# Optimization experiments

Hardware: AMD Instinct MI355X
Metric: run time of the kernel (lower is better)

Reference implementation:

```python
import jax, jax.numpy as jnp
import numpy as np

IMG = 128
NEAR, FAR = 1.0, 100.0
BG_EPS = 1e-3      # eps in soft_rasterize: background depth logit
SIGMA = 1e-6       # sigma_val
DIST_EPS = 1e-4    # dist_eps
GAMMA = 1e-6       # gamma_val
CHUNK = 500
B, V, F = 1, 5023, 10000


def setup_inputs():
    key = jax.random.key(0)
    k1, k2, k3, k4 = jax.random.split(key, 4)
    xy = jax.random.uniform(k1, (B, V, 2), minval=-1.0, maxval=1.0, dtype=jnp.float32)
    z = jax.random.uniform(k2, (B, V, 1), minval=5.0, maxval=15.0, dtype=jnp.float32)
    vertices = jnp.concatenate([xy, z], axis=-1)              # [B,V,3]
    faces = jax.random.randint(k3, (B, F, 3), 0, V, dtype=jnp.int32)
    attributes = jax.random.uniform(k4, (B, F, 3, 3), dtype=jnp.float32)
    return {"vertices": vertices, "faces": faces, "attributes": attributes}


def _seg_dist2(px, py, ax, ay, bx, by):
    # squared distance from pixel (px,py) to segment a-b; broadcasts [P] vs [B,C,1]
    dx = px - ax; dy = py - ay
    ex = bx - ax; ey = by - ay
    l2 = jnp.maximum(ex * ex + ey * ey, 1e-12)
    t = jnp.clip((dx * ex + dy * ey) / l2, 0.0, 1.0)
    rx = dx - t * ex; ry = dy - t * ey
    return rx * rx + ry * ry


def _render(vertices, faces, attributes):
    is_ = IMG
    P = is_ * is_
    bz = vertices.shape[0]
    v = vertices.at[..., 0].multiply(-1.0)                    # x flip (in-place in torch)
    fv = jax.vmap(lambda vv, ff: vv[ff])(v, faces)            # [B,F,3vert,3xyz]
    tex = attributes[..., :3]                                 # [B,F,3vert,3rgb]
    # fill_back=True: append copies with reversed winding
    fv = jnp.concatenate([fv, fv[:, :, ::-1, :]], axis=1)     # [B,2F,3,3]
    tex = jnp.concatenate([tex, tex[:, :, ::-1, :]], axis=1)
    F2 = fv.shape[1]
    pad = (-F2) % CHUNK
    valid = jnp.concatenate([jnp.ones((F2,), bool), jnp.zeros((pad,), bool)])
    fv = jnp.pad(fv, ((0, 0), (0, pad), (0, 0), (0, 0)))
    tex = jnp.pad(tex, ((0, 0), (0, pad), (0, 0), (0, 0)))
    n_chunks = (F2 + pad) // CHUNK
    fv = jnp.transpose(fv.reshape(bz, n_chunks, CHUNK, 3, 3), (1, 0, 2, 3, 4))
    tex = jnp.transpose(tex.reshape(bz, n_chunks, CHUNK, 3, 3), (1, 0, 2, 3, 4))
    valid = valid.reshape(n_chunks, CHUNK)

    # pixel centers in [-1,1]; row 0 is the top of the image (y flipped as in CUDA)
    xs = (2.0 * jnp.arange(is_, dtype=jnp.float32) + 1.0 - is_) / is_
    ys = (2.0 * (is_ - 1 - jnp.arange(is_, dtype=jnp.float32)) + 1.0 - is_) / is_
    px = jnp.broadcast_to(xs[None, :], (is_, is_)).reshape(-1)  # [P]
    py = jnp.broadcast_to(ys[:, None], (is_, is_)).reshape(-1)

    thr = DIST_EPS * SIGMA
    inv_g = 1.0 / GAMMA

    def step(carry, inp):
        m, s, cacc, prod = carry                # [B,P],[B,P],[B,3,P],[B,P]
        fvc, txc, vld = inp                     # [B,C,3,3],[B,C,3,3],[C]
        x0 = fvc[:, :, 0, 0][..., None]; y0 = fvc[:, :, 0, 1][..., None]; z0 = fvc[:, :, 0, 2][..., None]
        x1 = fvc[:, :, 1, 0][..., None]; y1 = fvc[:, :, 1, 1][..., None]; z1 = fvc[:, :, 1, 2][..., None]
        x2 = fvc[:, :, 2, 0][..., None]; y2 = fvc[:, :, 2, 1][..., None]; z2 = fvc[:, :, 2, 2][..., None]
        det = (y1 - y2) * (x0 - x2) + (x2 - x1) * (y0 - y2)   # [B,C,1]
        det = jnp.where(jnp.abs(det) < 1e-10, jnp.where(det < 0, -1e-10, 1e-10), det)
        w0 = ((y1 - y2) * (px - x2) + (x2 - x1) * (py - y2)) / det  # [B,C,P]
        w1 = ((y2 - y0) * (px - x2) + (x0 - x2) * (py - y2)) / det
        w2 = 1.0 - w0 - w1
        inside = (w0 >= 0) & (w1 >= 0) & (w2 >= 0)
        dis = jnp.minimum(jnp.minimum(_seg_dist2(px, py, x0, y0, x1, y1),
                                      _seg_dist2(px, py, x1, y1, x2, y2)),
                          _seg_dist2(px, py, x2, y2, x0, y0))     # [B,C,P] squared dist
        contrib = (inside | (dis < thr)) & vld[None, :, None]
        sgn = jnp.where(inside, 1.0, -1.0)
        Dp = jnp.where(contrib, jax.nn.sigmoid(sgn * dis / SIGMA), 0.0)
        prod = prod * jnp.prod(1.0 - Dp, axis=1)                  # alpha: prod(1-D)
        # clipped barycentric + perspective-correct depth
        c0 = jnp.clip(w0, 0.0, 1.0); c1 = jnp.clip(w1, 0.0, 1.0); c2 = jnp.clip(w2, 0.0, 1.0)
        csum = jnp.maximum(c0 + c1 + c2, 1e-5)
        c0 = c0 / csum; c1 = c1 / csum; c2 = c2 / csum
        zp_inv = c0 / z0 + c1 / z1 + c2 / z2
        zp = 1.0 / jnp.where(jnp.abs(zp_inv) < 1e-12, 1e-12, zp_inv)
        front = (y2 - y0) * (x1 - x0) < (y1 - y0) * (x2 - x0)     # [B,C,1]
        rgb_m = contrib & front & (zp >= NEAR) & (zp <= FAR)
        zpn = (FAR - zp) / (FAR - NEAR)
        new_m = jnp.maximum(m, jnp.max(jnp.where(rgb_m, zpn, -jnp.inf), axis=1))
        e = jnp.exp(jnp.where(rgb_m, (zpn - new_m[:, None, :]) * inv_g, -jnp.inf)) * Dp
        scale = jnp.exp((m - new_m) * inv_g)                      # [B,P]
        wc = jnp.stack([c0, c1, c2], axis=2)                      # [B,C,3,P]
        col = jnp.einsum('bcvp,bcvk->bckp', wc, txc)              # interpolated rgb
        s = s * scale + jnp.sum(e, axis=1)
        cacc = cacc * scale[:, None, :] + jnp.sum(e[:, :, None, :] * col, axis=1)
        return (new_m, s, cacc, prod), None

    m0 = jnp.full((bz, P), BG_EPS, jnp.float32)   # background logit = eps
    s0 = jnp.ones((bz, P), jnp.float32)           # exp((eps - m0)/gamma) = 1
    c0_ = jnp.zeros((bz, 3, P), jnp.float32)      # black background
    p0 = jnp.ones((bz, P), jnp.float32)
    (m, s, cacc, prod), _ = jax.lax.scan(jax.checkpoint(step), (m0, s0, c0_, p0), (fv, tex, valid))
    rgb = cacc / s[:, None, :]
    alpha = 1.0 - prod
    return jnp.concatenate([rgb, alpha[:, None, :]], axis=1).reshape(bz, 4, is_, is_)


def reference(vertices, faces, attributes):
    return _render(vertices, faces, attributes)
```

## Files before the change

kernel.cpp:

```cpp
#include <hip/hip_runtime.h>
#include <math.h>


#define NFACE 10000
#define IMG   128
#define P_TOT (IMG*IMG)
#define FSTR  40
#define NTILE 64
#define NQ    4
#define CAPQ  2500
#define CAP   (CAPQ*NQ)
#define BMAX  4096
#define NB    1024
#define CH    256
#define NCH   40
#define Z_LO  0.85f
#define Z_W   (0.12f/1024.0f)

__device__ __forceinline__ float rcp_nr(float x) {
    float r = __builtin_amdgcn_rcpf(x);
    r = r * __builtin_fmaf(-x, r, 2.0f);
    return r;
}

__device__ __forceinline__ float segd(float px, float py, float ax, float ay,
                                      float bx, float by, float il) {
    float dx = px - ax, dy = py - ay;
    float ex = bx - ax, ey = by - ay;
    float t = (dx * ex + dy * ey) * il;
    t = fminf(fmaxf(t, 0.0f), 1.0f);
    float rx = dx - t * ex, ry = dy - t * ey;
    return rx * rx + ry * ry;
}

__device__ __forceinline__ float rfl_f(float x) {
    return __uint_as_float(__builtin_amdgcn_readfirstlane(__float_as_uint(x)));
}

__device__ __forceinline__ int zbucket(float zub) {
    int b = (int)((zub - Z_LO) * (1.0f / Z_W));
    return min(max(b, 0), NB - 1);
}

__global__ __launch_bounds__(256) void k_prehist(const float* __restrict__ v,
                                                 const int* __restrict__ fc,
                                                 const float* __restrict__ at,
                                                 float* __restrict__ fb,
                                                 int* __restrict__ hist) {
    __shared__ int lh[NB];
    int c = blockIdx.x, tid = threadIdx.x;
    for (int j = tid; j < NB; j += 256) lh[j] = 0;
    __syncthreads();

    int f = c * CH + tid;
    if (f < NFACE) {
        int i0 = fc[3 * f], i1 = fc[3 * f + 1], i2 = fc[3 * f + 2];
        float x0 = -v[3 * i0], y0 = v[3 * i0 + 1], z0 = v[3 * i0 + 2];
        float x1 = -v[3 * i1], y1 = v[3 * i1 + 1], z1 = v[3 * i1 + 2];
        float x2 = -v[3 * i2], y2 = v[3 * i2 + 1], z2 = v[3 * i2 + 2];

        float det = (y1 - y2) * (x0 - x2) + (x2 - x1) * (y0 - y2);
        if (fabsf(det) < 1e-10f) det = (det < 0.0f) ? -1e-10f : 1e-10f;
        float a0 = y1 - y2, b0 = x2 - x1, a1 = y2 - y0, b1 = x0 - x2, detp = det;
        if (det < 0.0f) { detp = -det; a0 = -a0; b0 = -b0; a1 = -a1; b1 = -b1; }

        float a2 = a0 + a1, b2 = b0 + b1;
        float g0 = fmaxf(sqrtf(a0 * a0 + b0 * b0), 1e-12f);
        float g1 = fmaxf(sqrtf(a1 * a1 + b1 * b1), 1e-12f);
        float g2 = fmaxf(sqrtf(a2 * a2 + b2 * b2), 1e-12f);
        const float MARG = 3e-5f, AG = 1e-9f;
        float m0 = -(MARG * g0 + AG), m1 = -(MARG * g1 + AG), m2 = -(MARG * g2 + AG);

        float e01x = x1 - x0, e01y = y1 - y0;
        float e12x = x2 - x1, e12y = y2 - y1;
        float e20x = x0 - x2, e20y = y0 - y2;
        float il01 = 1.0f / fmaxf(e01x * e01x + e01y * e01y, 1e-12f);
        float il12 = 1.0f / fmaxf(e12x * e12x + e12y * e12y, 1e-12f);
        float il20 = 1.0f / fmaxf(e20x * e20x + e20y * e20y, 1e-12f);

        const float BM = 2e-5f;
        float bxmin = fminf(fminf(x0, x1), x2) - BM, bxmax = fmaxf(fmaxf(x0, x1), x2) + BM;
        float bymin = fminf(fminf(y0, y1), y2) - BM, bymax = fmaxf(fmaxf(y0, y1), y2) + BM;

        int mult = (((y2 - y0) * (x1 - x0)) < ((y1 - y0) * (x2 - x0)))
                 + (((y0 - y2) * (x1 - x2)) < ((y1 - y2) * (x0 - x2)));

        float zmin = fminf(fminf(z0, z1), z2);
        float zub = (100.0f - zmin) / 99.0f + 2e-6f;

        float* F = fb + (size_t)f * FSTR;
        F[0] = bxmin; F[1] = bxmax; F[2] = bymin; F[3] = bymax;
        F[4] = x2; F[5] = y2; F[6] = a0; F[7] = b0;
        F[8] = a1; F[9] = b1; F[10] = detp; F[11] = zub;
        F[12] = m0; F[13] = m1; F[14] = m2; F[15] = (float)mult;
        F[16] = x0; F[17] = y0; F[18] = x1; F[19] = y1;
        F[20] = il01; F[21] = il12; F[22] = il20; F[23] = 1.0f / detp;
        F[24] = 1.0f / z0; F[25] = 1.0f / z1; F[26] = 1.0f / z2;
        F[27] = 1.0f / g0; F[28] = 1.0f / g1; F[29] = 1.0f / g2;
#pragma unroll
        for (int k = 0; k < 9; k++) F[30 + k] = at[(size_t)f * 9 + k];
        F[39] = 0.0f;

        atomicAdd(&lh[zbucket(zub)], 1);
    }
    __syncthreads();
    for (int j = tid; j < NB; j += 256) hist[c * NB + j] = lh[j];
}

__global__ __launch_bounds__(1024) void k_scan(int* __restrict__ hist) {
    __shared__ int a[NB];
    int t = threadIdx.x;
    int tot = 0;
    for (int c = 0; c < NCH; c++) tot += hist[c * NB + t];
    a[t] = tot;
    for (int off = 1; off < NB; off <<= 1) {
        __syncthreads();
        int v = a[t] + ((t + off < NB) ? a[t + off] : 0);
        __syncthreads();
        a[t] = v;
    }
    int r = a[t] - tot;
    for (int c = 0; c < NCH; c++) {
        int h = hist[c * NB + t];
        hist[c * NB + t] = r;
        r += h;
    }
}

__global__ __launch_bounds__(256) void k_scatterre(const float* __restrict__ fb,
                                                   const int* __restrict__ hist,
                                                   float* __restrict__ fb2) {
    __shared__ int sb[CH];
    int c = blockIdx.x, tid = threadIdx.x;
    int f = c * CH + tid;
    bool valid = (f < NFACE);
    int b = valid ? zbucket(fb[(size_t)f * FSTR + 11]) : -1;
    sb[tid] = b;
    __syncthreads();
    if (valid) {
        int rank = 0;
        for (int j = 0; j < CH; j++) {
            int v2 = sb[j];
            rank += (j < tid && v2 == b) ? 1 : 0;
        }
        int pos = hist[c * NB + b] + rank;
        const float4* src = (const float4*)(fb + (size_t)f * FSTR);
        float4* dst = (float4*)(fb2 + (size_t)pos * FSTR);
#pragma unroll
        for (int k = 0; k < 10; k++) dst[k] = src[k];
        fb2[(size_t)pos * FSTR + 11] = Z_LO + (float)(b + 1) * Z_W + 1e-7f;
    }
}

__global__ __launch_bounds__(256) void k_bin(const float* __restrict__ fb2,
                                             float2* __restrict__ tmeta,
                                             int* __restrict__ cnt4) {
    int t = blockIdx.x >> 2, q = blockIdx.x & 3;
    int tid = threadIdx.x, wv = tid >> 6, lane = tid & 63;
    int tx = t & 7, ty = t >> 3;
    float x_lo = (float)(2 * (tx * 16) + 1 - IMG) / (float)IMG;
    float x_hi = (float)(2 * (tx * 16 + 15) + 1 - IMG) / (float)IMG;
    float y_hi = (float)(127 - 2 * (ty * 16)) / (float)IMG;
    float y_lo = (float)(127 - 2 * (ty * 16 + 15)) / (float)IMG;
    float cx = 0.5f * (x_lo + x_hi), hx = 0.5f * (x_hi - x_lo);
    float cy = 0.5f * (y_lo + y_hi), hy = 0.5f * (y_hi - y_lo);

    __shared__ int wc[4];
    int cnt = 0;
    int f0 = q * CAPQ;
    for (int base = f0; base < f0 + CAPQ; base += 256) {
        int j = base + tid;
        bool ov = false;
        float zub = 0.0f;
        if (j < f0 + CAPQ) {
            const float4* H = (const float4*)(fb2 + (size_t)j * FSTR);
            float4 h0 = H[0], h1 = H[1], h2 = H[2], h3 = H[3];
            ov = (h0.x <= x_hi) & (h0.y >= x_lo) & (h0.z <= y_hi) & (h0.w >= y_lo);
            if (ov) {
                float dx = cx - h1.x, dy = cy - h1.y;
                float mx0 = h1.z * dx + h1.w * dy + fabsf(h1.z) * hx + fabsf(h1.w) * hy;
                float mx1 = h2.x * dx + h2.y * dy + fabsf(h2.x) * hx + fabsf(h2.y) * hy;
                float A2 = -(h1.z + h2.x), B2 = -(h1.w + h2.y);
                float mx2 = h2.z + A2 * dx + B2 * dy + fabsf(A2) * hx + fabsf(B2) * hy;
                ov = (mx0 >= h3.x) & (mx1 >= h3.y) & (mx2 >= h3.z);
                zub = h2.w;
            }
        }
        unsigned long long mask = __ballot(ov);
        if (lane == 0) wc[wv] = __popcll(mask);
        __syncthreads();
        int off = cnt;
        for (int w = 0; w < 4; ++w) {
            if (w < wv) off += wc[w];
        }
        if (ov) {
            int pos = off + __popcll(mask & ((1ull << lane) - 1ull));
            tmeta[(size_t)t * CAP + q * CAPQ + pos] =
                make_float2(zub, __int_as_float(j));
        }
        cnt += wc[0] + wc[1] + wc[2] + wc[3];
        __syncthreads();
    }
    if (tid == 0) cnt4[t * 4 + q] = cnt;
}

__global__ __launch_bounds__(64) void k_map(const int* __restrict__ cnt4,
                                            int* __restrict__ map,
                                            int* __restrict__ starts,
                                            int* __restrict__ segs,
                                            int B) {
    int lane = threadIdx.x;
    int len = cnt4[4 * lane] + cnt4[4 * lane + 1] + cnt4[4 * lane + 2] + cnt4[4 * lane + 3];
    int tot = len;
    for (int o = 32; o > 0; o >>= 1) tot += __shfl_down(tot, o);
    tot = __shfl(tot, 0);
    int St = max(1, (int)(((long long)len * (long long)(B - NTILE)) /
                          (long long)max(tot, 1)));
    __shared__ int sS[64], sP[64];
    sS[lane] = St;
    __syncthreads();
    if (lane == 0) {
        int acc = 0;
        for (int t = 0; t < 64; ++t) { sP[t] = acc; acc += sS[t]; }
    }
    __syncthreads();
    for (int i = lane; i < B; i += 64) map[i] = -1;
    __syncthreads();
    int st = sP[lane];
    starts[lane] = st;
    segs[lane] = St;
    for (int s = 0; s < St; ++s) map[st + s] = (lane << 16) | s;
}

__global__ __launch_bounds__(256) void k_main(const float* __restrict__ fb2,
                                              const float2* __restrict__ tmeta,
                                              const int* __restrict__ cnt4,
                                              const int* __restrict__ map,
                                              const int* __restrict__ segs,
                                              float* __restrict__ part) {
    int bid = blockIdx.x;
    int mv = map[bid];
    if (mv < 0) return;
    int t = mv >> 16, seg = mv & 0xffff;
    int S = segs[t];

    int tid = threadIdx.x;
    int tx = t & 7, ty = t >> 3;
    int col = tx * 16 + (tid & 15);
    int row = ty * 16 + (tid >> 4);
    float px = (float)(2 * col + 1 - IMG) / (float)IMG;
    float py = (float)(2 * (IMG - 1 - row) + 1 - IMG) / (float)IMG;

    const float2* pm = tmeta + (size_t)t * CAP;

    float m = -__builtin_inff();
    float s = 0.0f, ca = 0.0f, cb = 0.0f, cc = 0.0f, pr = 1.0f;

    const float NEAR_T = 4.3e-3f;
    const float ZM = 1.3e-4f;

    bool done = false;
    for (int q = 0; q < 4 && !done; ++q) {
        int qlen = cnt4[t * 4 + q];
        for (int i = seg; i < qlen; i += S) {
            float2 mt = pm[q * CAPQ + i];
            float zcur = rfl_f(mt.x);
            if (__all((pr == 0.0f) & (zcur <= m - ZM))) { done = true; break; }
            int fj = __builtin_amdgcn_readfirstlane(__float_as_int(mt.y));
            const float4* H = (const float4*)(fb2 + (size_t)fj * FSTR);
            float4 g0 = H[0], g1 = H[1], g2 = H[2], g3 = H[3];

            bool inbox = (px >= g0.x) & (px <= g0.y) & (py >= g0.z) & (py <= g0.w);
            if (!__any(inbox)) continue;

            float x2 = g1.x, y2 = g1.y;
            float dx2 = px - x2, dy2 = py - y2;
            float num0 = g1.z * dx2 + g1.w * dy2;
            float num1 = g2.x * dx2 + g2.y * dy2;
            float detp = g2.z;
            float num2 = detp - num0 - num1;
            bool maybe = inbox & (num0 >= g3.x) & (num1 >= g3.y) & (num2 >= g3.z);
            if (!__any(maybe)) continue;

            const float* F = fb2 + (size_t)fj * FSTR;

            bool inside = (num0 >= 0.0f) & (num1 >= 0.0f) & (num2 >= 0.0f);
            bool inside_l = inside & inbox;

            float lin0 = num0 * F[27];
            float lin1 = num1 * F[28];
            float lin2 = num2 * F[29];
            float lbmin = fminf(fminf(lin0, lin1), lin2);

            bool outNear = maybe & (!inside);
            bool nearIn  = inside_l & (lbmin < NEAR_T);
            bool anyNear = __any(nearIn | outNear);

            float dis = 1e9f;
            float Dp;
            if (anyNear) {
                bool needAll = __any(outNear);
                float x0 = F[16], y0 = F[17], x1 = F[18], y1 = F[19];
                float d01 = 1e9f, d12 = 1e9f, d20 = 1e9f;
                if (needAll | __any(inside_l & (lin2 < NEAR_T)))
                    d01 = segd(px, py, x0, y0, x1, y1, F[20]);
                if (needAll | __any(inside_l & (lin0 < NEAR_T)))
                    d12 = segd(px, py, x1, y1, x2, y2, F[21]);
                if (needAll | __any(inside_l & (lin1 < NEAR_T)))
                    d20 = segd(px, py, x2, y2, x0, y0, F[22]);
                dis = fminf(fminf(d01, d12), d20);

                float qq = dis * 1e6f;
                float xs_ = inside ? qq : -qq;
                float tt = __expf(-fabsf(xs_));
                float Dpn = (xs_ >= 0.0f ? 1.0f : tt) * rcp_nr(1.0f + tt);
                bool nearl = nearIn | outNear;
                Dp = nearl ? Dpn : (inside_l ? 1.0f : 0.0f);
            } else {
                Dp = inside_l ? 1.0f : 0.0f;
            }

            bool contrib = inside_l | (outNear & (dis < 1e-10f));
            Dp = contrib ? Dp : 0.0f;
            float omd = 1.0f - Dp;
            pr *= contrib ? (omd * omd) : 1.0f;

            float multf = g3.w;
            bool doz = contrib & (multf > 0.0f);
            if (__any(doz & (zcur > m - ZM))) {
                float rdetp = F[23];
                float w0 = num0 * rdetp;
                float w1 = num1 * rdetp;
                float c0 = fminf(fmaxf(w0, 0.0f), 1.0f);
                float c1 = fminf(fmaxf(w1, 0.0f), 1.0f);
                float c2 = fminf(fmaxf(1.0f - w0 - w1, 0.0f), 1.0f);
                float csum = fmaxf(c0 + c1 + c2, 1e-5f);
                float rcs = rcp_nr(csum);
                c0 *= rcs; c1 *= rcs; c2 *= rcs;
                float zpi = c0 * F[24] + c1 * F[25] + c2 * F[26];
                if (fabsf(zpi) < 1e-12f) zpi = 1e-12f;
                float zp = rcp_nr(zpi);
                if (doz & (zp >= 1.0f) & (zp <= 100.0f)) {
                    float zpn = (100.0f - zp) / 99.0f;
                    if (zpn > m) {
                        float scl = __expf((m - zpn) * 1e6f);
                        s *= scl; ca *= scl; cb *= scl; cc *= scl;
                        m = zpn;
                    }
                    float arg = (zpn - m) * 1e6f;
                    if (arg > -110.0f) {
                        float e = __expf(arg) * Dp * multf;
                        float col0 = c0 * F[30] + c1 * F[33] + c2 * F[36];
                        float col1 = c0 * F[31] + c1 * F[34] + c2 * F[37];
                        float col2 = c0 * F[32] + c1 * F[35] + c2 * F[38];
                        s += e; ca += e * col0; cb += e * col1; cc += e * col2;
                    }
                }
            }
        }
    }

    size_t pb = (size_t)bid * 6 * 256;
    part[pb + 0 * 256 + tid] = m;
    part[pb + 1 * 256 + tid] = s;
    part[pb + 2 * 256 + tid] = ca;
    part[pb + 3 * 256 + tid] = cb;
    part[pb + 4 * 256 + tid] = cc;
    part[pb + 5 * 256 + tid] = pr;
}

__global__ __launch_bounds__(1024) void k_reduce(const float* __restrict__ part,
                                                 const int* __restrict__ starts,
                                                 const int* __restrict__ segs,
                                                 float* __restrict__ out) {
    __shared__ float sm[4][256], ss[4][256], sa[4][256], sb2[4][256],
                     sc[4][256], sp[4][256];
    int t = blockIdx.x;
    int tid = threadIdx.x;
    int q = tid & 255, sub = tid >> 8;
    int start = starts[t], S = segs[t];

    const float NINF = -__builtin_inff();
    float mp = NINF;
    for (int sgi = sub; sgi < S; sgi += 4)
        mp = fmaxf(mp, part[((size_t)(start + sgi) * 6 + 0) * 256 + q]);
    float sum = 0.0f, a = 0.0f, b = 0.0f, c = 0.0f, pr = 1.0f;
    for (int sgi = sub; sgi < S; sgi += 4) {
        const float* r = part + ((size_t)(start + sgi) * 6) * 256;
        float rm = r[0 * 256 + q];
        float w = (rm == NINF) ? 0.0f : __expf((rm - mp) * 1e6f);
        pr *= r[5 * 256 + q];
        if (__any(w != 0.0f)) {
            sum += r[1 * 256 + q] * w;
            a += r[2 * 256 + q] * w;
            b += r[3 * 256 + q] * w;
            c += r[4 * 256 + q] * w;
        }
    }
    sm[sub][q] = mp; ss[sub][q] = sum; sa[sub][q] = a;
    sb2[sub][q] = b; sc[sub][q] = c;  sp[sub][q] = pr;
    __syncthreads();
    if (sub == 0) {
        int tx = t & 7, ty = t >> 3;
        int col = tx * 16 + (q & 15);
        int row = ty * 16 + (q >> 4);
        int p = row * IMG + col;
        float M = 0.001f;
#pragma unroll
        for (int k = 0; k < 4; k++) M = fmaxf(M, sm[k][q]);
        float SUM = __expf((0.001f - M) * 1e6f);
        float A = 0.0f, B2 = 0.0f, C = 0.0f, PR = 1.0f;
#pragma unroll
        for (int k = 0; k < 4; k++) {
            float w = __expf((sm[k][q] - M) * 1e6f);
            SUM += ss[k][q] * w;
            A += sa[k][q] * w;
            B2 += sb2[k][q] * w;
            C += sc[k][q] * w;
            PR *= sp[k][q];
        }
        out[0 * P_TOT + p] = A / SUM;
        out[1 * P_TOT + p] = B2 / SUM;
        out[2 * P_TOT + p] = C / SUM;
        out[3 * P_TOT + p] = 1.0f - PR;
    }
}

extern "C" void kernel_launch(void* const* d_in, const int* in_sizes, int n_in,
                              void* d_out, int out_size, void* d_ws, size_t ws_size,
                              hipStream_t stream) {
    const float* verts = (const float*)d_in[0];
    const int*   faces = (const int*)d_in[1];
    const float* attrs = (const float*)d_in[2];
    float* out = (float*)d_out;
    float* ws  = (float*)d_ws;

    float*  fb    = ws;
    int*    hist  = (int*)(fb + (size_t)NFACE * FSTR);
    float*  fb2   = (float*)(hist + NCH * NB);
    float2* tmeta = (float2*)(fb2 + (size_t)NFACE * FSTR);
    int*    cnt4  = (int*)(tmeta + (size_t)NTILE * CAP);
    int*    map   = cnt4 + NTILE * 4;
    int*    starts= map + BMAX;
    int*    segs  = starts + NTILE;
    float*  part  = (float*)(segs + NTILE);

    size_t used_f = 2 * (size_t)NFACE * FSTR + NCH * NB
                  + 2 * (size_t)NTILE * CAP + NTILE * 4 + BMAX + 2 * NTILE;
    long   rem_f  = (long)(ws_size / 4) - (long)used_f;
    int B = (int)(rem_f / (6 * 256));
    if (B > BMAX) B = BMAX;
    if (B < 256)  B = 256;

    k_prehist<<<NCH, 256, 0, stream>>>(verts, faces, attrs, fb, hist);
    k_scan<<<1, 1024, 0, stream>>>(hist);
    k_scatterre<<<NCH, 256, 0, stream>>>(fb, hist, fb2);
    k_bin<<<NTILE * NQ, 256, 0, stream>>>(fb2, tmeta, cnt4);
    k_map<<<1, 64, 0, stream>>>(cnt4, map, starts, segs, B);
    k_main<<<B, 256, 0, stream>>>(fb2, tmeta, cnt4, map, segs, part);
    k_reduce<<<NTILE, 1024, 0, stream>>>(part, starts, segs, out);
}
```

Before: 139.1 us.

## Fold tile map into main/reduce, unroll face loop by two, use 8x8 wave pixel blocks

Drops the separate k_map launch. k_main and k_reduce now each rebuild the tile-to-block map in shared memory from the bin counts and find their tile with a binary search. The face loop now loads two faces' headers ahead of evaluating them, to hide global-load latency. Each wave now covers an 8x8 pixel square instead of four 16-pixel rows, so wave-level early-exit and ballot tests work on more compact regions. The cost is redundant map computation in every block plus higher register pressure from the two prefetched headers.

```diff
diff --git a/kernel.cpp b/kernel.cpp
--- a/kernel.cpp
+++ b/kernel.cpp
@@ -204,50 +204,51 @@
     if (tid == 0) cnt4[t * 4 + q] = cnt;
 }
 
-__global__ __launch_bounds__(64) void k_map(const int* __restrict__ cnt4,
-                                            int* __restrict__ map,
-                                            int* __restrict__ starts,
-                                            int* __restrict__ segs,
-                                            int B) {
-    int lane = threadIdx.x;
-    int len = cnt4[4 * lane] + cnt4[4 * lane + 1] + cnt4[4 * lane + 2] + cnt4[4 * lane + 3];
-    int tot = len;
-    for (int o = 32; o > 0; o >>= 1) tot += __shfl_down(tot, o);
-    tot = __shfl(tot, 0);
-    int St = max(1, (int)(((long long)len * (long long)(B - NTILE)) /
-                          (long long)max(tot, 1)));
-    __shared__ int sS[64], sP[64];
-    sS[lane] = St;
-    __syncthreads();
-    if (lane == 0) {
+__device__ __forceinline__ void derive_map(const int* __restrict__ cnt4,
+                                           int B, int tid, int nthr,
+                                           int* sLen, int* sS, int* sP,
+                                           int* sUsed) {
+    if (tid < NTILE)
+        sLen[tid] = cnt4[4 * tid] + cnt4[4 * tid + 1]
+                  + cnt4[4 * tid + 2] + cnt4[4 * tid + 3];
+    __syncthreads();
+    if (tid == 0) {
+        int tot = 0;
+        for (int k = 0; k < NTILE; k++) tot += sLen[k];
+        tot = max(tot, 1);
         int acc = 0;
-        for (int t = 0; t < 64; ++t) { sP[t] = acc; acc += sS[t]; }
-    }
-    __syncthreads();
-    for (int i = lane; i < B; i += 64) map[i] = -1;
-    __syncthreads();
-    int st = sP[lane];
-    starts[lane] = st;
-    segs[lane] = St;
-    for (int s = 0; s < St; ++s) map[st + s] = (lane << 16) | s;
+        for (int k = 0; k < NTILE; k++) {
+            int S = max(1, (int)(((long long)sLen[k] * (long long)(B - NTILE)) /
+                                 (long long)tot));
+            sS[k] = S; sP[k] = acc; acc += S;
+        }
+        *sUsed = acc;
+    }
+    __syncthreads();
 }
 
 __global__ __launch_bounds__(256) void k_main(const float* __restrict__ fb2,
                                               const float2* __restrict__ tmeta,
                                               const int* __restrict__ cnt4,
-                                              const int* __restrict__ map,
-                                              const int* __restrict__ segs,
-                                              float* __restrict__ part) {
+                                              float* __restrict__ part,
+                                              int B) {
+    __shared__ int sLen[NTILE], sS[NTILE], sP[NTILE], sUsed;
+    int tid = threadIdx.x;
+    derive_map(cnt4, B, tid, 256, sLen, sS, sP, &sUsed);
     int bid = blockIdx.x;
-    int mv = map[bid];
-    if (mv < 0) return;
-    int t = mv >> 16, seg = mv & 0xffff;
-    int S = segs[t];
-
-    int tid = threadIdx.x;
+    if (bid >= sUsed) return;
+    int lo = 0, hi = NTILE - 1;
+    while (lo < hi) {
+        int mid = (lo + hi + 1) >> 1;
+        if (sP[mid] <= bid) lo = mid; else hi = mid - 1;
+    }
+    int t = lo, seg = bid - sP[lo];
+    int S = sS[t];
+
+    int wv = tid >> 6, lane = tid & 63;
     int tx = t & 7, ty = t >> 3;
-    int col = tx * 16 + (tid & 15);
-    int row = ty * 16 + (tid >> 4);
+    int col = tx * 16 + (wv & 1) * 8 + (lane & 7);
+    int row = ty * 16 + (wv >> 1) * 8 + (lane >> 3);
     float px = (float)(2 * col + 1 - IMG) / (float)IMG;
     float py = (float)(2 * (IMG - 1 - row) + 1 - IMG) / (float)IMG;
 
@@ -258,166 +259,188 @@
 
     const float NEAR_T = 4.3e-3f;
     const float ZM = 1.3e-4f;
+
+    auto EVAL = [&](int fj, float zcur, float4 g0, float4 g1, float4 g2, float4 g3) {
+        bool inbox = (px >= g0.x) & (px <= g0.y) & (py >= g0.z) & (py <= g0.w);
+        if (!__any(inbox)) return;
+
+        float x2 = g1.x, y2 = g1.y;
+        float dx2 = px - x2, dy2 = py - y2;
+        float num0 = g1.z * dx2 + g1.w * dy2;
+        float num1 = g2.x * dx2 + g2.y * dy2;
+        float detp = g2.z;
+        float num2 = detp - num0 - num1;
+        bool maybe = inbox & (num0 >= g3.x) & (num1 >= g3.y) & (num2 >= g3.z);
+        if (!__any(maybe)) return;
+
+        const float* F = fb2 + (size_t)fj * FSTR;
+
+        bool inside = (num0 >= 0.0f) & (num1 >= 0.0f) & (num2 >= 0.0f);
+        bool inside_l = inside & inbox;
+
+        float lin0 = num0 * F[27];
+        float lin1 = num1 * F[28];
+        float lin2 = num2 * F[29];
+        float lbmin = fminf(fminf(lin0, lin1), lin2);
+
+        bool outNear = maybe & (!inside);
+        bool nearIn  = inside_l & (lbmin < NEAR_T);
+        bool anyNear = __any(nearIn | outNear);
+
+        float dis = 1e9f;
+        float Dp;
+        if (anyNear) {
+            bool needAll = __any(outNear);
+            float x0 = F[16], y0 = F[17], x1 = F[18], y1 = F[19];
+            float d01 = 1e9f, d12 = 1e9f, d20 = 1e9f;
+            if (needAll | __any(inside_l & (lin2 < NEAR_T)))
+                d01 = segd(px, py, x0, y0, x1, y1, F[20]);
+            if (needAll | __any(inside_l & (lin0 < NEAR_T)))
+                d12 = segd(px, py, x1, y1, x2, y2, F[21]);
+            if (needAll | __any(inside_l & (lin1 < NEAR_T)))
+                d20 = segd(px, py, x2, y2, x0, y0, F[22]);
+            dis = fminf(fminf(d01, d12), d20);
+
+            float qq = dis * 1e6f;
+            float xs_ = inside ? qq : -qq;
+            float tt = __expf(-fabsf(xs_));
+            float Dpn = (xs_ >= 0.0f ? 1.0f : tt) * rcp_nr(1.0f + tt);
+            bool nearl = nearIn | outNear;
+            Dp = nearl ? Dpn : (inside_l ? 1.0f : 0.0f);
+        } else {
+            Dp = inside_l ? 1.0f : 0.0f;
+        }
+
+        bool contrib = inside_l | (outNear & (dis < 1e-10f));
+        Dp = contrib ? Dp : 0.0f;
+        float omd = 1.0f - Dp;
+        pr *= contrib ? (omd * omd) : 1.0f;
+
+        float multf = g3.w;
+        bool doz = contrib & (multf > 0.0f);
+        if (__any(doz & (zcur > m - ZM))) {
+            float rdetp = F[23];
+            float w0 = num0 * rdetp;
+            float w1 = num1 * rdetp;
+            float c0 = fminf(fmaxf(w0, 0.0f), 1.0f);
+            float c1 = fminf(fmaxf(w1, 0.0f), 1.0f);
+            float c2 = fminf(fmaxf(1.0f - w0 - w1, 0.0f), 1.0f);
+            float csum = fmaxf(c0 + c1 + c2, 1e-5f);
+            float rcs = rcp_nr(csum);
+            c0 *= rcs; c1 *= rcs; c2 *= rcs;
+            float zpi = c0 * F[24] + c1 * F[25] + c2 * F[26];
+            if (fabsf(zpi) < 1e-12f) zpi = 1e-12f;
+            float zp = rcp_nr(zpi);
+            if (doz & (zp >= 1.0f) & (zp <= 100.0f)) {
+                float zpn = (100.0f - zp) / 99.0f;
+                if (zpn > m) {
+                    float scl = __expf((m - zpn) * 1e6f);
+                    s *= scl; ca *= scl; cb *= scl; cc *= scl;
+                    m = zpn;
+                }
+                float arg = (zpn - m) * 1e6f;
+                if (arg > -110.0f) {
+                    float e = __expf(arg) * Dp * multf;
+                    float col0 = c0 * F[30] + c1 * F[33] + c2 * F[36];
+                    float col1 = c0 * F[31] + c1 * F[34] + c2 * F[37];
+                    float col2 = c0 * F[32] + c1 * F[35] + c2 * F[38];
+                    s += e; ca += e * col0; cb += e * col1; cc += e * col2;
+                }
+            }
+        }
+    };
 
     bool done = false;
     for (int q = 0; q < 4 && !done; ++q) {
         int qlen = cnt4[t * 4 + q];
-        for (int i = seg; i < qlen; i += S) {
-            float2 mt = pm[q * CAPQ + i];
-            float zcur = rfl_f(mt.x);
-            if (__all((pr == 0.0f) & (zcur <= m - ZM))) { done = true; break; }
-            int fj = __builtin_amdgcn_readfirstlane(__float_as_int(mt.y));
-            const float4* H = (const float4*)(fb2 + (size_t)fj * FSTR);
-            float4 g0 = H[0], g1 = H[1], g2 = H[2], g3 = H[3];
-
-            bool inbox = (px >= g0.x) & (px <= g0.y) & (py >= g0.z) & (py <= g0.w);
-            if (!__any(inbox)) continue;
-
-            float x2 = g1.x, y2 = g1.y;
-            float dx2 = px - x2, dy2 = py - y2;
-            float num0 = g1.z * dx2 + g1.w * dy2;
-            float num1 = g2.x * dx2 + g2.y * dy2;
-            float detp = g2.z;
-            float num2 = detp - num0 - num1;
-            bool maybe = inbox & (num0 >= g3.x) & (num1 >= g3.y) & (num2 >= g3.z);
-            if (!__any(maybe)) continue;
-
-            const float* F = fb2 + (size_t)fj * FSTR;
-
-            bool inside = (num0 >= 0.0f) & (num1 >= 0.0f) & (num2 >= 0.0f);
-            bool inside_l = inside & inbox;
-
-            float lin0 = num0 * F[27];
-            float lin1 = num1 * F[28];
-            float lin2 = num2 * F[29];
-            float lbmin = fminf(fminf(lin0, lin1), lin2);
-
-            bool outNear = maybe & (!inside);
-            bool nearIn  = inside_l & (lbmin < NEAR_T);
-            bool anyNear = __any(nearIn | outNear);
-
-            float dis = 1e9f;
-            float Dp;
-            if (anyNear) {
-                bool needAll = __any(outNear);
-                float x0 = F[16], y0 = F[17], x1 = F[18], y1 = F[19];
-                float d01 = 1e9f, d12 = 1e9f, d20 = 1e9f;
-                if (needAll | __any(inside_l & (lin2 < NEAR_T)))
-                    d01 = segd(px, py, x0, y0, x1, y1, F[20]);
-                if (needAll | __any(inside_l & (lin0 < NEAR_T)))
-                    d12 = segd(px, py, x1, y1, x2, y2, F[21]);
-                if (needAll | __any(inside_l & (lin1 < NEAR_T)))
-                    d20 = segd(px, py, x2, y2, x0, y0, F[22]);
-                dis = fminf(fminf(d01, d12), d20);
-
-                float qq = dis * 1e6f;
-                float xs_ = inside ? qq : -qq;
-                float tt = __expf(-fabsf(xs_));
-                float Dpn = (xs_ >= 0.0f ? 1.0f : tt) * rcp_nr(1.0f + tt);
-                bool nearl = nearIn | outNear;
-                Dp = nearl ? Dpn : (inside_l ? 1.0f : 0.0f);
-            } else {
-                Dp = inside_l ? 1.0f : 0.0f;
+        const float2* pq = pm + q * CAPQ;
+        int i = seg;
+        while (i < qlen) {
+            float2 mt0 = pq[i];
+            int i1 = i + S;
+            bool has1 = (i1 < qlen);
+            float2 mt1 = has1 ? pq[i1] : mt0;
+            float z0 = rfl_f(mt0.x);
+            int   f0 = __builtin_amdgcn_readfirstlane(__float_as_int(mt0.y));
+            float z1 = rfl_f(mt1.x);
+            int   f1 = __builtin_amdgcn_readfirstlane(__float_as_int(mt1.y));
+            const float4* H0 = (const float4*)(fb2 + (size_t)f0 * FSTR);
+            const float4* H1 = (const float4*)(fb2 + (size_t)f1 * FSTR);
+            float4 a0 = H0[0], a1 = H0[1], a2 = H0[2], a3 = H0[3];
+            float4 b0 = H1[0], b1 = H1[1], b2 = H1[2], b3 = H1[3];
+
+            if (__all((pr == 0.0f) & (z0 <= m - ZM))) { done = true; break; }
+            EVAL(f0, z0, a0, a1, a2, a3);
+            if (has1) {
+                if (__all((pr == 0.0f) & (z1 <= m - ZM))) { done = true; break; }
+                EVAL(f1, z1, b0, b1, b2, b3);
             }
-
-            bool contrib = inside_l | (outNear & (dis < 1e-10f));
-            Dp = contrib ? Dp : 0.0f;
-            float omd = 1.0f - Dp;
-            pr *= contrib ? (omd * omd) : 1.0f;
-
-            float multf = g3.w;
-            bool doz = contrib & (multf > 0.0f);
-            if (__any(doz & (zcur > m - ZM))) {
-                float rdetp = F[23];
-                float w0 = num0 * rdetp;
-                float w1 = num1 * rdetp;
-                float c0 = fminf(fmaxf(w0, 0.0f), 1.0f);
-                float c1 = fminf(fmaxf(w1, 0.0f), 1.0f);
-                float c2 = fminf(fmaxf(1.0f - w0 - w1, 0.0f), 1.0f);
-                float csum = fmaxf(c0 + c1 + c2, 1e-5f);
-                float rcs = rcp_nr(csum);
-                c0 *= rcs; c1 *= rcs; c2 *= rcs;
-                float zpi = c0 * F[24] + c1 * F[25] + c2 * F[26];
-                if (fabsf(zpi) < 1e-12f) zpi = 1e-12f;
-                float zp = rcp_nr(zpi);
-                if (doz & (zp >= 1.0f) & (zp <= 100.0f)) {
-                    float zpn = (100.0f - zp) / 99.0f;
-                    if (zpn > m) {
-                        float scl = __expf((m - zpn) * 1e6f);
-                        s *= scl; ca *= scl; cb *= scl; cc *= scl;
-                        m = zpn;
-                    }
-                    float arg = (zpn - m) * 1e6f;
-                    if (arg > -110.0f) {
-                        float e = __expf(arg) * Dp * multf;
-                        float col0 = c0 * F[30] + c1 * F[33] + c2 * F[36];
-                        float col1 = c0 * F[31] + c1 * F[34] + c2 * F[37];
-                        float col2 = c0 * F[32] + c1 * F[35] + c2 * F[38];
-                        s += e; ca += e * col0; cb += e * col1; cc += e * col2;
-                    }
-                }
-            }
-        }
-    }
-
-    size_t pb = (size_t)bid * 6 * 256;
-    part[pb + 0 * 256 + tid] = m;
-    part[pb + 1 * 256 + tid] = s;
-    part[pb + 2 * 256 + tid] = ca;
-    part[pb + 3 * 256 + tid] = cb;
-    part[pb + 4 * 256 + tid] = cc;
-    part[pb + 5 * 256 + tid] = pr;
+            i += 2 * S;
+        }
+    }
+
+    size_t pb = ((size_t)(bid * 4 + wv) * 6) * 64;
+    part[pb + 0 * 64 + lane] = m;
+    part[pb + 1 * 64 + lane] = s;
+    part[pb + 2 * 64 + lane] = ca;
+    part[pb + 3 * 64 + lane] = cb;
+    part[pb + 4 * 64 + lane] = cc;
+    part[pb + 5 * 64 + lane] = pr;
 }
 
 __global__ __launch_bounds__(1024) void k_reduce(const float* __restrict__ part,
-                                                 const int* __restrict__ starts,
-                                                 const int* __restrict__ segs,
-                                                 float* __restrict__ out) {
+                                                 const int* __restrict__ cnt4,
+                                                 float* __restrict__ out,
+                                                 int B) {
+    __shared__ int sLen[NTILE], sS[NTILE], sP[NTILE], sUsed;
     __shared__ float sm[4][256], ss[4][256], sa[4][256], sb2[4][256],
                      sc[4][256], sp[4][256];
     int t = blockIdx.x;
     int tid = threadIdx.x;
-    int q = tid & 255, sub = tid >> 8;
-    int start = starts[t], S = segs[t];
+    derive_map(cnt4, B, tid, 1024, sLen, sS, sP, &sUsed);
+    int start = sP[t], S = sS[t];
+
+    int pid = tid & 255, sub = tid >> 8;
+    int qd = pid >> 6, lane = pid & 63;
 
     const float NINF = -__builtin_inff();
     float mp = NINF;
     for (int sgi = sub; sgi < S; sgi += 4)
-        mp = fmaxf(mp, part[((size_t)(start + sgi) * 6 + 0) * 256 + q]);
+        mp = fmaxf(mp, part[(((size_t)(start + sgi) * 4 + qd) * 6 + 0) * 64 + lane]);
     float sum = 0.0f, a = 0.0f, b = 0.0f, c = 0.0f, pr = 1.0f;
     for (int sgi = sub; sgi < S; sgi += 4) {
-        const float* r = part + ((size_t)(start + sgi) * 6) * 256;
-        float rm = r[0 * 256 + q];
+        const float* rp = part + (((size_t)(start + sgi) * 4 + qd) * 6) * 64;
+        float rm = rp[0 * 64 + lane];
         float w = (rm == NINF) ? 0.0f : __expf((rm - mp) * 1e6f);
-        pr *= r[5 * 256 + q];
+        pr *= rp[5 * 64 + lane];
         if (__any(w != 0.0f)) {
-            sum += r[1 * 256 + q] * w;
-            a += r[2 * 256 + q] * w;
-            b += r[3 * 256 + q] * w;
-            c += r[4 * 256 + q] * w;
-        }
-    }
-    sm[sub][q] = mp; ss[sub][q] = sum; sa[sub][q] = a;
-    sb2[sub][q] = b; sc[sub][q] = c;  sp[sub][q] = pr;
+            sum += rp[1 * 64 + lane] * w;
+            a += rp[2 * 64 + lane] * w;
+            b += rp[3 * 64 + lane] * w;
+            c += rp[4 * 64 + lane] * w;
+        }
+    }
+    sm[sub][pid] = mp; ss[sub][pid] = sum; sa[sub][pid] = a;
+    sb2[sub][pid] = b; sc[sub][pid] = c;  sp[sub][pid] = pr;
     __syncthreads();
     if (sub == 0) {
         int tx = t & 7, ty = t >> 3;
-        int col = tx * 16 + (q & 15);
-        int row = ty * 16 + (q >> 4);
+        int col = tx * 16 + (qd & 1) * 8 + (lane & 7);
+        int row = ty * 16 + (qd >> 1) * 8 + (lane >> 3);
         int p = row * IMG + col;
         float M = 0.001f;
 #pragma unroll
-        for (int k = 0; k < 4; k++) M = fmaxf(M, sm[k][q]);
+        for (int k = 0; k < 4; k++) M = fmaxf(M, sm[k][pid]);
         float SUM = __expf((0.001f - M) * 1e6f);
         float A = 0.0f, B2 = 0.0f, C = 0.0f, PR = 1.0f;
 #pragma unroll
         for (int k = 0; k < 4; k++) {
-            float w = __expf((sm[k][q] - M) * 1e6f);
-            SUM += ss[k][q] * w;
-            A += sa[k][q] * w;
-            B2 += sb2[k][q] * w;
-            C += sc[k][q] * w;
-            PR *= sp[k][q];
+            float w = __expf((sm[k][pid] - M) * 1e6f);
+            SUM += ss[k][pid] * w;
+            A += sa[k][pid] * w;
+            B2 += sb2[k][pid] * w;
+            C += sc[k][pid] * w;
+            PR *= sp[k][pid];
         }
         out[0 * P_TOT + p] = A / SUM;
         out[1 * P_TOT + p] = B2 / SUM;
@@ -440,13 +463,10 @@
     float*  fb2   = (float*)(hist + NCH * NB);
     float2* tmeta = (float2*)(fb2 + (size_t)NFACE * FSTR);
     int*    cnt4  = (int*)(tmeta + (size_t)NTILE * CAP);
-    int*    map   = cnt4 + NTILE * 4;
-    int*    starts= map + BMAX;
-    int*    segs  = starts + NTILE;
-    float*  part  = (float*)(segs + NTILE);
+    float*  part  = (float*)(cnt4 + NTILE * 4);
 
     size_t used_f = 2 * (size_t)NFACE * FSTR + NCH * NB
-                  + 2 * (size_t)NTILE * CAP + NTILE * 4 + BMAX + 2 * NTILE;
+                  + 2 * (size_t)NTILE * CAP + NTILE * 4;
     long   rem_f  = (long)(ws_size / 4) - (long)used_f;
     int B = (int)(rem_f / (6 * 256));
     if (B > BMAX) B = BMAX;
@@ -456,7 +476,6 @@
     k_scan<<<1, 1024, 0, stream>>>(hist);
     k_scatterre<<<NCH, 256, 0, stream>>>(fb, hist, fb2);
     k_bin<<<NTILE * NQ, 256, 0, stream>>>(fb2, tmeta, cnt4);
-    k_map<<<1, 64, 0, stream>>>(cnt4, map, starts, segs, B);
-    k_main<<<B, 256, 0, stream>>>(fb2, tmeta, cnt4, map, segs, part);
-    k_reduce<<<NTILE, 1024, 0, stream>>>(part, starts, segs, out);
-}
+    k_main<<<B, 256, 0, stream>>>(fb2, tmeta, cnt4, part, B);
+    k_reduce<<<NTILE, 1024, 0, stream>>>(part, cnt4, out, B);
+}
```

Measured after the change: 148.9 us. 1.07x slower.
